# Optimization experiments

Hardware: AMD Instinct MI355X
Metric: run time of the kernel (lower is better)

Reference implementation:

```python
import jax, jax.numpy as jnp
import numpy as np

NUM_CODES = 1024
CODE_DIM = 256
COMMITMENT_COST = 0.25
B, T = 32, 1024


def setup_inputs() -> dict:
    key = jax.random.key(0)
    k1, k2 = jax.random.split(key)
    latents = jax.random.normal(k1, (B, CODE_DIM, T), dtype=jnp.float32)
    # faithful to nn.Embedding init uniform_(-1/num_codes, 1/num_codes)
    codebook = jax.random.uniform(k2, (NUM_CODES, CODE_DIM), dtype=jnp.float32,
                                  minval=-1.0 / NUM_CODES, maxval=1.0 / NUM_CODES)
    return {"latents": latents, "codebook": codebook}


def reference(latents, codebook):
    # latents: [B, D, T], codebook: [K, D]
    b, d, t = latents.shape
    flat = jnp.transpose(latents, (0, 2, 1)).reshape(-1, d)  # [B*T, D]
    distances = (jnp.sum(flat * flat, axis=1, keepdims=True)
                 - 2.0 * flat @ codebook.T
                 + jnp.sum(codebook * codebook, axis=1))  # [B*T, K]
    indices = jnp.argmin(distances, axis=1)  # [B*T]
    quantized = codebook[indices].reshape(b, t, d).transpose(0, 2, 1)  # [B, D, T]
    codebook_loss = jnp.mean((quantized - jax.lax.stop_gradient(latents)) ** 2)
    commitment_loss = jnp.mean((jax.lax.stop_gradient(quantized) - latents) ** 2)
    loss = codebook_loss + COMMITMENT_COST * commitment_loss
    # straight-through estimator
    quantized_st = latents + jax.lax.stop_gradient(quantized - latents)
    return quantized_st, loss, indices.reshape(b, t)
```

## Files before the change

kernel.cpp:

```cpp
#include <hip/hip_runtime.h>
#include <math.h>

#define Dd 256
#define Tt 1024
#define Bb 32
#define Kk 1024
#define NROWS (Bb*Tt)
#define OUTQ  (Bb*Dd*Tt)
#define KP   512
#define SLACK 4e-4f
#define LIST_CAP 458752u
#define CANDB_CAP 1024u

typedef __bf16 b16x8 __attribute__((ext_vector_type(8)));
typedef float  f32x4 __attribute__((ext_vector_type(4)));

#define OFF_LOSS  0
#define OFF_GCNT  8
#define OFF_W2    256
#define OFF_X2    8192
#define OFF_IDX   139264
#define OFF_PACK  270336
#define OFF_GMIN  532480
#define OFF_RMING 663552
#define OFF_LIST  1712128
#define OFF_BT    5382144
#define OFF_X     6430720
#define OFF_A     39985152
#define MIN_WS    (OFF_A + (size_t)NROWS*KP*2)

__device__ __forceinline__ void gload16(const void* g, void* l) {
    __builtin_amdgcn_global_load_lds(
        (const __attribute__((address_space(1))) void*)g,
        (__attribute__((address_space(3))) void*)l, 16, 0, 0);
}

__global__ void vq_w2(const float* __restrict__ cb, float* __restrict__ w2f) {
#pragma clang fp contract(off)
    const int k = blockIdx.x * 256 + threadIdx.x;
    if (k >= Kk) return;
    const float* w = cb + (size_t)k * Dd;
    float h[2];
    for (int half = 0; half < 2; ++half) {
        const float* p = w + half * 128;
        float r[8];
        for (int j = 0; j < 8; ++j) { float v = p[j]; r[j] = v * v; }
        for (int m = 1; m < 16; ++m)
            for (int j = 0; j < 8; ++j) { float v = p[m*8 + j]; r[j] += v * v; }
        h[half] = ((r[0]+r[1]) + (r[2]+r[3])) + ((r[4]+r[5]) + (r[6]+r[7]));
    }
    w2f[k] = h[0] + h[1];
}

__global__ void vq_prep_bt(const float* __restrict__ cb, __bf16* __restrict__ BT) {
    const int c = blockIdx.x, t = threadIdx.x;
    float v = cb[(size_t)c*Dd + t];
    __bf16 hi = (__bf16)v;
    BT[(size_t)c*KP + t]       = hi;
    BT[(size_t)c*KP + 256 + t] = hi;
}

__global__ void vq_prep_a(const float* __restrict__ lat, float* __restrict__ X,
                          __bf16* __restrict__ A) {
    __shared__ float tl[64][65];
    const int tid = threadIdx.x;
    const int rowbase = blockIdx.x * 64;
    const int b = rowbase >> 10, t0 = rowbase & 1023;
    const int d0 = blockIdx.y * 64;
    const int tt = tid & 63, sub = tid >> 6;
#pragma unroll
    for (int it = 0; it < 16; ++it) {
        int d = it*4 + sub;
        tl[d][tt] = lat[((size_t)(b*Dd + d0 + d))*Tt + t0 + tt];
    }
    __syncthreads();
    const int dd = tid & 63;
#pragma unroll
    for (int it = 0; it < 16; ++it) {
        int t = it*4 + sub;
        float v = tl[dd][t];
        int grow = rowbase + t;
        X[(size_t)grow*Dd + d0 + dd] = v;
        __bf16 hi = (__bf16)v;
        __bf16 lo = (__bf16)(v - (float)hi);
        size_t ab = (size_t)grow*KP + d0 + dd;
        A[ab]       = hi;
        A[ab + 256] = lo;
    }
}

__global__ __launch_bounds__(256) void vq_x2(const float* __restrict__ X,
                                             float* __restrict__ x2f) {
    __shared__ float xrow[4][256];
    const int tid = threadIdx.x;
    const int wv = tid >> 6, l = tid & 63;
    const int row = blockIdx.x * 4 + wv;

    const float4* xg = (const float4*)(X + (size_t)row * Dd);
    *(float4*)&xrow[wv][l*4] = xg[l];
    __syncthreads();

    float s = 0.0f;
    if (l < 16) {
#pragma clang fp contract(off)
        const int h = l >> 3, j = l & 7;
        float v = xrow[wv][h*128 + j];
        float r8 = v * v;
        for (int m = 1; m < 16; ++m) {
            v = xrow[wv][h*128 + m*8 + j];
            r8 += v * v;
        }
        s = r8;
    }
    s += __shfl_xor(s, 1, 64);
    s += __shfl_xor(s, 2, 64);
    s += __shfl_xor(s, 4, 64);
    s += __shfl_xor(s, 8, 64);
    if (l == 0) x2f[row] = s;
}

__global__ __launch_bounds__(256) void vq_gemm(const __bf16* __restrict__ A,
                                               const __bf16* __restrict__ BT,
                                               const float* __restrict__ w2f,
                                               unsigned* __restrict__ gcnt,
                                               uint2* __restrict__ list,
                                               float* __restrict__ rming) {
    __shared__ __align__(16) char smem[32768];
    __bf16* As = (__bf16*)smem;
    __bf16* Bs = (__bf16*)(smem + 16384);
    float (*rminS)[2] = (float(*)[2])smem;
    unsigned* nCand   = (unsigned*)(smem + 1024);
    unsigned* baseS   = (unsigned*)(smem + 1032);
    unsigned* candRC  = (unsigned*)(smem + 2048);
    float*    candF   = (float*)(smem + 6144);

    const int tid = threadIdx.x;
    const int bm = blockIdx.x, bn = blockIdx.y;
    const int l = tid & 63, wv = tid >> 6;
    const int wm = (wv & 1) * 64, wn = (wv >> 1) * 64;
    const int m16 = l & 15, quad = l >> 4;

    f32x4 acc[4][4];
#pragma unroll
    for (int i = 0; i < 4; ++i)
#pragma unroll
        for (int j = 0; j < 4; ++j) acc[i][j] = (f32x4){0.f,0.f,0.f,0.f};

    const int r8  = l >> 3;
    const int c8  = l & 7;
    const int csw = ((c8 ^ r8) * 8);
    const int sw  = m16 & 7;

    for (int kt = 0; kt < 8; ++kt) {
        const int k0 = kt * 64;
#pragma unroll
        for (int p = 0; p < 4; ++p) {
            const int R0 = wv*32 + p*8;
            gload16(&A [(size_t)(bm*128 + R0 + r8)*KP + k0 + csw], &As[R0*64]);
            gload16(&BT[(size_t)(bn*128 + R0 + r8)*KP + k0 + csw], &Bs[R0*64]);
        }
        __syncthreads();
#pragma unroll
        for (int ks = 0; ks < 64; ks += 32) {
            const int k8 = ks >> 3;
            b16x8 a[4], b[4];
#pragma unroll
            for (int i = 0; i < 4; ++i) {
                const int row = wm + 16*i + m16;
                a[i] = *(const b16x8*)((const char*)As + row*128 + (((k8 + quad) ^ sw) * 16));
            }
#pragma unroll
            for (int j = 0; j < 4; ++j) {
                const int row = wn + 16*j + m16;
                b[j] = *(const b16x8*)((const char*)Bs + row*128 + (((k8 + quad) ^ sw) * 16));
            }
#pragma unroll
            for (int i = 0; i < 4; ++i)
#pragma unroll
                for (int j = 0; j < 4; ++j)
                    acc[i][j] = __builtin_amdgcn_mfma_f32_16x16x32_bf16(a[i], b[j], acc[i][j], 0, 0, 0);
        }
        __syncthreads();
    }

    float w2n[4];
#pragma unroll
    for (int j = 0; j < 4; ++j) w2n[j] = w2f[bn*128 + wn + 16*j + m16];

    float vmin[4][4];
#pragma unroll
    for (int i = 0; i < 4; ++i)
#pragma unroll
        for (int g = 0; g < 4; ++g) {
            float v = w2n[0] - 2.0f * acc[i][0][g];
#pragma unroll
            for (int j = 1; j < 4; ++j)
                v = fminf(v, w2n[j] - 2.0f * acc[i][j][g]);
#pragma unroll
            for (int off = 1; off <= 8; off <<= 1)
                v = fminf(v, __shfl_xor(v, off, 64));
            vmin[i][g] = v;
        }
    if (m16 == 0) {
#pragma unroll
        for (int i = 0; i < 4; ++i)
#pragma unroll
            for (int g = 0; g < 4; ++g)
                rminS[wm + 16*i + quad*4 + g][wn >> 6] = vmin[i][g];
    }
    if (tid == 0) *nCand = 0u;
    __syncthreads();
    if (tid < 128)
        rming[((size_t)(bm*128 + tid))*8 + bn] = fminf(rminS[tid][0], rminS[tid][1]);
#pragma unroll
    for (int i = 0; i < 4; ++i)
#pragma unroll
        for (int g = 0; g < 4; ++g) {
            const int rloc = wm + 16*i + quad*4 + g;
            const float thr = fminf(rminS[rloc][0], rminS[rloc][1]) + SLACK;
#pragma unroll
            for (int j = 0; j < 4; ++j) {
                float f = w2n[j] - 2.0f * acc[i][j][g];
                if (f <= thr) {
                    unsigned slot = atomicAdd(nCand, 1u);
                    if (slot < CANDB_CAP) {
                        candRC[slot] = ((unsigned)(bm*128 + rloc) << 10)
                                     | (unsigned)(bn*128 + wn + 16*j + m16);
                        candF[slot]  = f;
                    }
                }
            }
        }
    __syncthreads();
    unsigned nc = *nCand; if (nc > CANDB_CAP) nc = CANDB_CAP;
    if (tid == 0) *baseS = atomicAdd(gcnt, nc);
    __syncthreads();
    const unsigned base = *baseS;
    for (unsigned i = tid; i < nc; i += 256) {
        unsigned dst = base + i;
        if (dst < LIST_CAP) {
            uint2 e; e.x = candRC[i]; e.y = __float_as_uint(candF[i]);
            list[dst] = e;
        }
    }
}

__global__ __launch_bounds__(256) void vq_gmin(const float* __restrict__ rming,
                                               float* __restrict__ gmin) {
    const int row = blockIdx.x * 256 + threadIdx.x;
    const float4* p = (const float4*)(rming + (size_t)row * 8);
    float4 a = p[0], b = p[1];
    float m = fminf(fminf(fminf(a.x, a.y), fminf(a.z, a.w)),
                    fminf(fminf(b.x, b.y), fminf(b.z, b.w)));
    gmin[row] = m + SLACK;
}

__global__ __launch_bounds__(256) void vq_rescore(const float* __restrict__ X,
                                                  const float* __restrict__ cb,
                                                  const float* __restrict__ w2f,
                                                  const float* __restrict__ x2f,
                                                  const float* __restrict__ gmin,
                                                  const unsigned* __restrict__ gcnt,
                                                  const uint2* __restrict__ list,
                                                  unsigned long long* __restrict__ pack) {
    unsigned n = *gcnt; if (n > LIST_CAP) n = LIST_CAP;
    const unsigned stride = gridDim.x * 256u;
    for (unsigned i = blockIdx.x * 256u + threadIdx.x; i < n; i += stride) {
        const uint2 e = list[i];
        const int row = (int)(e.x >> 10);
        const int c   = (int)(e.x & 1023u);
        if (__uint_as_float(e.y) > gmin[row]) continue;

        const float4* wq = (const float4*)(cb + (size_t)c * Dd);
        const float4* xq = (const float4*)(X + (size_t)row * Dd);
        float acc = 0.0f;
#pragma unroll 8
        for (int m = 0; m < 64; ++m) {
            float4 xa = xq[m], wa = wq[m];
            acc = __builtin_fmaf(xa.x, wa.x, acc);
            acc = __builtin_fmaf(xa.y, wa.y, acc);
            acc = __builtin_fmaf(xa.z, wa.z, acc);
            acc = __builtin_fmaf(xa.w, wa.w, acc);
        }
        float t2 = x2f[row] - 2.0f * acc;
        float dv = t2 + w2f[c];
        unsigned long long pk = ((unsigned long long)__float_as_uint(dv) << 32)
                              | (unsigned long long)(unsigned)c;
        atomicMin(&pack[row], pk);
    }
}

__global__ __launch_bounds__(256) void vq_pick(const unsigned long long* __restrict__ pack,
                                               int* __restrict__ idx,
                                               double* __restrict__ loss_acc) {
    __shared__ double wsum[4];
    const int tid = threadIdx.x;
    const int row = blockIdx.x * 256 + tid;
    const unsigned long long pk = pack[row];
    idx[row] = (int)(pk & 0xFFFFFFFFull);
    double d = (double)__uint_as_float((unsigned)(pk >> 32));
    for (int off = 32; off; off >>= 1) d += __shfl_xor(d, off, 64);
    if ((tid & 63) == 0) wsum[tid >> 6] = d;
    __syncthreads();
    if (tid == 0) atomicAdd(loss_acc, wsum[0] + wsum[1] + wsum[2] + wsum[3]);
}

typedef float float8_t __attribute__((ext_vector_type(8)));
__global__ __launch_bounds__(512) void vq_main(const float* __restrict__ latents,
                                               const float* __restrict__ cb,
                                               const float* __restrict__ w2f,
                                               int* __restrict__ idx,
                                               double* __restrict__ loss_acc) {
    __shared__ float  xs[Dd*64];
    __shared__ float  x2f[64];
    __shared__ float  bsd[8*64];
    __shared__ int    bci[8*64];
    __shared__ double red[64];
    const int tid = threadIdx.x;
    const int rr  = tid & 63;
    const int dg  = tid >> 6;
    const int blk = blockIdx.x;
    const int bb  = blk >> 4;
    const int t0  = (blk & 15) << 6;
    const float* lat = latents + (size_t)bb * Dd * Tt + t0;
    for (int d = dg; d < Dd; d += 8) xs[d*64 + rr] = lat[(size_t)d * Tt + rr];
    __syncthreads();
    if (tid < 64) {
#pragma clang fp contract(off)
        float h[2];
        for (int half = 0; half < 2; ++half) {
            float r[8];
            for (int j = 0; j < 8; ++j) { float v = xs[(half*128 + j)*64 + tid]; r[j] = v*v; }
            for (int m = 1; m < 16; ++m)
                for (int j = 0; j < 8; ++j) { float v = xs[(half*128 + m*8 + j)*64 + tid]; r[j] += v*v; }
            h[half] = ((r[0]+r[1]) + (r[2]+r[3])) + ((r[4]+r[5]) + (r[6]+r[7]));
        }
        x2f[tid] = h[0] + h[1];
    }
    __syncthreads();
    const int slab = __builtin_amdgcn_readfirstlane(tid >> 6);
    const int lane = tid & 63;
    const float x2r = x2f[lane];
    const float* wq = cb + (size_t)slab * 128 * Dd;
    float best = 3.4e38f; int bestc = 0;
    for (int cg = 0; cg < 16; ++cg) {
        const int c0 = cg * 8;
        float acc[8];
#pragma unroll
        for (int g = 0; g < 8; ++g) acc[g] = 0.0f;
        for (int kc = 0; kc < 32; ++kc) {
            float8_t w8[8];
#pragma unroll
            for (int g = 0; g < 8; ++g) w8[g] = *(const float8_t*)(wq + (size_t)(c0+g)*Dd + kc*8);
            float xk[8];
#pragma unroll
            for (int j = 0; j < 8; ++j) xk[j] = xs[(kc*8 + j)*64 + lane];
#pragma unroll
            for (int g = 0; g < 8; ++g)
#pragma unroll
                for (int j = 0; j < 8; ++j) acc[g] = __builtin_fmaf(xk[j], w8[g][j], acc[g]);
        }
#pragma unroll
        for (int g = 0; g < 8; ++g) {
            float t2 = x2r - 2.0f * acc[g];
            float dvv = t2 + w2f[slab*128 + c0 + g];
            if (dvv < best) { best = dvv; bestc = slab*128 + c0 + g; }
        }
    }
    bsd[slab*64 + lane] = best; bci[slab*64 + lane] = bestc;
    __syncthreads();
    if (tid < 64) {
        float b0 = bsd[tid]; int ci = bci[tid];
#pragma unroll
        for (int s = 1; s < 8; ++s) { float b1 = bsd[s*64 + tid]; if (b1 < b0) { b0 = b1; ci = bci[s*64 + tid]; } }
        idx[blk*64 + tid] = ci; red[tid] = (double)b0;
    }
    __syncthreads();
    if (tid == 0) { double s = 0.0; for (int i = 0; i < 64; ++i) s += red[i]; atomicAdd(loss_acc, s); }
}

__global__ void vq_gather(const float* __restrict__ cb,
                          const int* __restrict__ idx,
                          float* __restrict__ out) {
    const size_t g = (size_t)blockIdx.x * 256 + threadIdx.x;
    const int t  = (int)(g & 1023);
    const int d4 = (int)((g >> 10) & 63);
    const int b  = (int)(g >> 16);
    const int i  = idx[b*Tt + t];
    const float4 w4 = *(const float4*)(cb + (size_t)i*Dd + d4*4);
    float* o = out + ((size_t)(b*Dd + d4*4)) * Tt + t;
    o[0]    = w4.x;
    o[Tt]   = w4.y;
    o[2*Tt] = w4.z;
    o[3*Tt] = w4.w;
}

__global__ void vq_finalize(const int* __restrict__ idx,
                            const double* __restrict__ loss_acc,
                            float* __restrict__ out) {
    const int r = blockIdx.x * 256 + threadIdx.x;
    if (r < NROWS) out[OUTQ + 1 + r] = (float)idx[r];
    if (r == 0)    out[OUTQ] = (float)(1.25 * loss_acc[0] / (double)OUTQ);
}

extern "C" void kernel_launch(void* const* d_in, const int* in_sizes, int n_in,
                              void* d_out, int out_size, void* d_ws, size_t ws_size,
                              hipStream_t stream) {
    const float* latents = (const float*)d_in[0];
    const float* cb      = (const float*)d_in[1];
    float* out = (float*)d_out;
    char*  ws  = (char*)d_ws;

    double* loss = (double*)(ws + OFF_LOSS);
    float*  w2f  = (float*)(ws + OFF_W2);
    int*    idx  = (int*)(ws + OFF_IDX);

    hipMemsetAsync(ws, 0, 16, stream);
    vq_w2<<<4, 256, 0, stream>>>(cb, w2f);

    if (ws_size >= (size_t)MIN_WS) {
        unsigned*           gcnt  = (unsigned*)(ws + OFF_GCNT);
        float*              x2f   = (float*)(ws + OFF_X2);
        unsigned long long* pack  = (unsigned long long*)(ws + OFF_PACK);
        float*              gmin  = (float*)(ws + OFF_GMIN);
        float*              rming = (float*)(ws + OFF_RMING);
        uint2*              list  = (uint2*)(ws + OFF_LIST);
        __bf16*             BT    = (__bf16*)(ws + OFF_BT);
        float*              X     = (float*)(ws + OFF_X);
        __bf16*             A     = (__bf16*)(ws + OFF_A);

        hipMemsetAsync(pack, 0xFF, sizeof(unsigned long long) * NROWS, stream);
        vq_prep_bt<<<Kk, 256, 0, stream>>>(cb, BT);
        vq_prep_a<<<dim3(NROWS/64, 4), 256, 0, stream>>>(latents, X, A);
        vq_x2<<<NROWS/4, 256, 0, stream>>>(X, x2f);
        vq_gemm<<<dim3(NROWS/128, 8), 256, 0, stream>>>(A, BT, w2f, gcnt, list, rming);
        vq_gmin<<<NROWS/256, 256, 0, stream>>>(rming, gmin);
        vq_rescore<<<1024, 256, 0, stream>>>(X, cb, w2f, x2f, gmin, gcnt, list, pack);
        vq_pick<<<NROWS/256, 256, 0, stream>>>(pack, idx, loss);
    } else {
        vq_main<<<NROWS/64, 512, 0, stream>>>(latents, cb, w2f, idx, loss);
    }

    vq_gather<<<(Bb*(Dd/4)*Tt)/256, 256, 0, stream>>>(cb, idx, out);
    vq_finalize<<<(NROWS + 255)/256, 256, 0, stream>>>(idx, loss, out);
}
```

Baseline: 233.3 us.

## Double-buffer GEMM LDS tiles and fuse codebook norm into bf16 prep

The bf16 GEMM now keeps two LDS tile buffers, so the global-to-LDS load of the next K slice is issued before the MFMAs on the current slice run. This removes one barrier per iteration and aims to hide load latency. Shared memory grows to 64KB per block, which may lower occupancy. Separately, the codebook squared-norm computation is folded into the bf16 transpose prep kernel, dropping one launch on the fast path.

```diff
diff --git a/kernel.cpp b/kernel.cpp
--- a/kernel.cpp
+++ b/kernel.cpp
@@ -52,12 +52,36 @@
     w2f[k] = h[0] + h[1];
 }
 
-__global__ void vq_prep_bt(const float* __restrict__ cb, __bf16* __restrict__ BT) {
+__global__ __launch_bounds__(256) void vq_cbprep(const float* __restrict__ cb,
+                                                 float* __restrict__ w2f,
+                                                 __bf16* __restrict__ BT) {
+    __shared__ float wrow[256];
     const int c = blockIdx.x, t = threadIdx.x;
     float v = cb[(size_t)c*Dd + t];
+    wrow[t] = v;
     __bf16 hi = (__bf16)v;
     BT[(size_t)c*KP + t]       = hi;
     BT[(size_t)c*KP + 256 + t] = hi;
+    __syncthreads();
+    if (t < 64) {
+        float s = 0.0f;
+        if (t < 16) {
+#pragma clang fp contract(off)
+            const int h = t >> 3, j = t & 7;
+            float u = wrow[h*128 + j];
+            float r8 = u * u;
+            for (int m = 1; m < 16; ++m) {
+                u = wrow[h*128 + m*8 + j];
+                r8 += u * u;
+            }
+            s = r8;
+        }
+        s += __shfl_xor(s, 1, 64);
+        s += __shfl_xor(s, 2, 64);
+        s += __shfl_xor(s, 4, 64);
+        s += __shfl_xor(s, 8, 64);
+        if (t == 0) w2f[c] = s;
+    }
 }
 
 __global__ void vq_prep_a(const float* __restrict__ lat, float* __restrict__ X,
@@ -125,9 +149,7 @@
                                                unsigned* __restrict__ gcnt,
                                                uint2* __restrict__ list,
                                                float* __restrict__ rming) {
-    __shared__ __align__(16) char smem[32768];
-    __bf16* As = (__bf16*)smem;
-    __bf16* Bs = (__bf16*)(smem + 16384);
+    __shared__ __align__(16) char smem[65536];
     float (*rminS)[2] = (float(*)[2])smem;
     unsigned* nCand   = (unsigned*)(smem + 1024);
     unsigned* baseS   = (unsigned*)(smem + 1032);
@@ -150,38 +172,50 @@
     const int c8  = l & 7;
     const int csw = ((c8 ^ r8) * 8);
     const int sw  = m16 & 7;
-
-    for (int kt = 0; kt < 8; ++kt) {
+    const size_t abase = (size_t)(bm*128) * KP;
+    const size_t bbase = (size_t)(bn*128) * KP;
+
+    auto stage = [&](int kt, int bsel) {
+        char* dstA = smem + bsel*32768;
+        char* dstB = smem + bsel*32768 + 16384;
         const int k0 = kt * 64;
 #pragma unroll
         for (int p = 0; p < 4; ++p) {
             const int R0 = wv*32 + p*8;
-            gload16(&A [(size_t)(bm*128 + R0 + r8)*KP + k0 + csw], &As[R0*64]);
-            gload16(&BT[(size_t)(bn*128 + R0 + r8)*KP + k0 + csw], &Bs[R0*64]);
-        }
-        __syncthreads();
+            gload16(&A [abase + (size_t)(R0 + r8)*KP + k0 + csw], dstA + R0*128);
+            gload16(&BT[bbase + (size_t)(R0 + r8)*KP + k0 + csw], dstB + R0*128);
+        }
+    };
+    auto compute = [&](int bsel) {
+        const char* As = smem + bsel*32768;
+        const char* Bs = smem + bsel*32768 + 16384;
 #pragma unroll
         for (int ks = 0; ks < 64; ks += 32) {
             const int k8 = ks >> 3;
             b16x8 a[4], b[4];
 #pragma unroll
-            for (int i = 0; i < 4; ++i) {
-                const int row = wm + 16*i + m16;
-                a[i] = *(const b16x8*)((const char*)As + row*128 + (((k8 + quad) ^ sw) * 16));
-            }
-#pragma unroll
-            for (int j = 0; j < 4; ++j) {
-                const int row = wn + 16*j + m16;
-                b[j] = *(const b16x8*)((const char*)Bs + row*128 + (((k8 + quad) ^ sw) * 16));
-            }
+            for (int i = 0; i < 4; ++i)
+                a[i] = *(const b16x8*)(As + (wm + 16*i + m16)*128 + (((k8 + quad) ^ sw) * 16));
+#pragma unroll
+            for (int j = 0; j < 4; ++j)
+                b[j] = *(const b16x8*)(Bs + (wn + 16*j + m16)*128 + (((k8 + quad) ^ sw) * 16));
 #pragma unroll
             for (int i = 0; i < 4; ++i)
 #pragma unroll
                 for (int j = 0; j < 4; ++j)
                     acc[i][j] = __builtin_amdgcn_mfma_f32_16x16x32_bf16(a[i], b[j], acc[i][j], 0, 0, 0);
         }
+    };
+
+    stage(0, 0);
+    __syncthreads();
+#pragma unroll
+    for (int kt = 0; kt < 7; ++kt) {
+        stage(kt + 1, (kt + 1) & 1);
+        compute(kt & 1);
         __syncthreads();
     }
+    compute(1);
 
     float w2n[4];
 #pragma unroll
@@ -416,7 +450,6 @@
     int*    idx  = (int*)(ws + OFF_IDX);
 
     hipMemsetAsync(ws, 0, 16, stream);
-    vq_w2<<<4, 256, 0, stream>>>(cb, w2f);
 
     if (ws_size >= (size_t)MIN_WS) {
         unsigned*           gcnt  = (unsigned*)(ws + OFF_GCNT);
@@ -430,7 +463,7 @@
         __bf16*             A     = (__bf16*)(ws + OFF_A);
 
         hipMemsetAsync(pack, 0xFF, sizeof(unsigned long long) * NROWS, stream);
-        vq_prep_bt<<<Kk, 256, 0, stream>>>(cb, BT);
+        vq_cbprep<<<Kk, 256, 0, stream>>>(cb, w2f, BT);
         vq_prep_a<<<dim3(NROWS/64, 4), 256, 0, stream>>>(latents, X, A);
         vq_x2<<<NROWS/4, 256, 0, stream>>>(X, x2f);
         vq_gemm<<<dim3(NROWS/128, 8), 256, 0, stream>>>(A, BT, w2f, gcnt, list, rming);
@@ -438,6 +471,7 @@
         vq_rescore<<<1024, 256, 0, stream>>>(X, cb, w2f, x2f, gmin, gcnt, list, pack);
         vq_pick<<<NROWS/256, 256, 0, stream>>>(pack, idx, loss);
     } else {
+        vq_w2<<<4, 256, 0, stream>>>(cb, w2f);
         vq_main<<<NROWS/64, 512, 0, stream>>>(latents, cb, w2f, idx, loss);
     }
 
```

Result: faster. 222.6 us (-4.6%).
